# Performance work log

Hardware: AMD Instinct MI355X
Metric: run time of the kernel (lower is better)

## Reference

```python
import jax, jax.numpy as jnp
import numpy as np

HEADS = 8


def setup_inputs() -> dict:
    key = jax.random.key(0)
    ks = jax.random.split(key, 9)
    B, C, H, W = 16, 512, 32, 32
    d = C // HEADS
    scale = d ** -0.5
    return {
        "x": jax.random.normal(ks[0], (B, C, H, W), dtype=jnp.float32),
        "Wq": jax.random.normal(ks[1], (C, C), dtype=jnp.float32) * (C ** -0.5),
        "bq": jax.random.normal(ks[2], (C,), dtype=jnp.float32) * 0.02,
        "Wk": jax.random.normal(ks[3], (C, C), dtype=jnp.float32) * (C ** -0.5),
        "bk": jax.random.normal(ks[4], (C,), dtype=jnp.float32) * 0.02,
        "Wv": jax.random.normal(ks[5], (C, C), dtype=jnp.float32) * (C ** -0.5),
        "bv": jax.random.normal(ks[6], (C,), dtype=jnp.float32) * 0.02,
        "rel_h": jax.random.normal(ks[7], (d, H, 1), dtype=jnp.float32) * scale,
        "rel_w": jax.random.normal(ks[8], (d, 1, W), dtype=jnp.float32) * scale,
    }


def reference(x, Wq, bq, Wk, bk, Wv, bv, rel_h, rel_w):
    B, C, H, W = x.shape
    heads = HEADS
    d = C // heads
    scale = d ** -0.5
    N = H * W
    xf = x.reshape(B, C, N)  # 1x1 conv == per-pixel linear over channels
    q = (jnp.einsum('oc,bcn->bon', Wq, xf) + bq[:, None]).reshape(B, heads, d, N)
    k = (jnp.einsum('oc,bcn->bon', Wk, xf) + bk[:, None]).reshape(B, heads, d, N)
    v = (jnp.einsum('oc,bcn->bon', Wv, xf) + bv[:, None]).reshape(B, heads, d, N)
    q = q * scale
    # content-content scores [B, heads, N, N]
    cc = jnp.einsum('bhdi,bhdj->bhij', q, k)
    # relative position bias table [d, N], projected by q
    cp_tab = (rel_h + rel_w).reshape(d, N)
    cp = jnp.einsum('bhdi,dj->bhij', q, cp_tab)
    beta = jax.nn.softmax(cc + cp, axis=-1)
    attn = jnp.einsum('bhij,bhdj->bhid', beta, v)  # [B, heads, N, d]
    # original does .view(x.shape) on [b,h,i,d] -> keep same raw reshape
    return attn.reshape(B, C, H, W)
```

## Files before the change

kernel.cpp:

```cpp
#include <hip/hip_runtime.h>
#include <hip/hip_bf16.h>
#include <stdint.h>

typedef unsigned short u16;
typedef u16 u16x8 __attribute__((ext_vector_type(8)));
typedef u16 u16x4 __attribute__((ext_vector_type(4)));
typedef __bf16 bf16x8 __attribute__((ext_vector_type(8)));
typedef float f32x4 __attribute__((ext_vector_type(4)));

#define MFMA16(a, b, c) __builtin_amdgcn_mfma_f32_16x16x32_bf16((a), (b), (c), 0, 0, 0)

#define SCALE_Q 0.18033688011112042f

__device__ __forceinline__ u16 f2b(float f) {
    union { float f; unsigned u; } v; v.f = f;
    unsigned r = v.u + 0x7FFFu + ((v.u >> 16) & 1u);
    return (u16)(r >> 16);
}
__device__ __forceinline__ u16 f2b_h(float f) {
    union { float f; unsigned u; } v; v.f = f;
    return (u16)((v.u + 0x8000u) >> 16);
}

__global__ __launch_bounds__(256) void prep(
    const float* __restrict__ x,
    const float* __restrict__ Wq, const float* __restrict__ Wk,
    const float* __restrict__ Wv,
    u16* __restrict__ wb, u16* __restrict__ xT) {
    __shared__ __align__(16) u16 Ls[128 * 72];
    const int tid = threadIdx.x;

    if (blockIdx.x < 384) {
        int g = blockIdx.x * 256 + tid;
        int which = g >> 15;
        const float* src = which == 0 ? Wq : (which == 1 ? Wk : Wv);
        int off = (g & 32767) * 8;
        f32x4 a = *(const f32x4*)(src + off);
        f32x4 b = *(const f32x4*)(src + off + 4);
        u16x8 o;
#pragma unroll
        for (int i = 0; i < 4; ++i) { o[i] = f2b_h(a[i]); o[4 + i] = f2b_h(b[i]); }
        *(u16x8*)(wb + (size_t)g * 8) = o;
        return;
    }

    const int bid = blockIdx.x - 384;
    const int b  = bid >> 6;
    const int ct = (bid >> 3) & 7;
    const int nt = bid & 7;
    const int C0 = ct * 64, N0 = nt * 128;
    const float* xb = x + ((size_t)b << 19);

#pragma unroll
    for (int rep = 0; rep < 4; ++rep) {
        int id = tid + rep * 256;
        int oct = id >> 7, n = id & 127;
        const float* xp = xb + (size_t)(C0 + oct * 8) * 1024 + N0 + n;
        u16x8 xv;
#pragma unroll
        for (int k = 0; k < 8; ++k) xv[k] = f2b_h(xp[k * 1024]);
        *(u16x8*)(Ls + n * 72 + oct * 8) = xv;
    }
    __syncthreads();
#pragma unroll
    for (int rep = 0; rep < 4; ++rep) {
        int id = tid + rep * 256;
        int n = id >> 3, c8 = id & 7;
        *(u16x8*)(xT + ((size_t)b << 19) + (size_t)(N0 + n) * 512 + C0 + c8 * 8) =
            *(u16x8*)(Ls + n * 72 + c8 * 8);
    }
}

__global__ __launch_bounds__(256, 3) void qkv_proj(
    const u16* __restrict__ xT, const u16* __restrict__ wb,
    const float* __restrict__ bq, const float* __restrict__ bk,
    const float* __restrict__ bv,
    const float* __restrict__ rel_h, const float* __restrict__ rel_w,
    u16* __restrict__ qws, u16* __restrict__ kws, u16* __restrict__ vws) {
    __shared__ __align__(16) u16 Xs[128 * 72];
    __shared__ __align__(16) u16 Ws[128 * 72];

    const int tid  = threadIdx.x;
    const int wave = tid >> 6, lane = tid & 63;
    const int quad = lane >> 4, l16 = lane & 15;
    const int wr = wave >> 1, wc = wave & 1;

    const int id = blockIdx.x;
    const int nt = id & 7;
    const int r  = id >> 3;
    const int o0 = r & 3;
    const int r2 = r >> 2;
    const int mm = r2 % 3;
    const int b  = r2 / 3;
    const int N0 = nt * 128;
    const int O0 = o0 * 128;

    const u16*   W    = wb + (size_t)mm * 262144;
    const float* bias = mm == 0 ? bq : (mm == 1 ? bk : bv);
    const u16*   Xb   = xT + ((size_t)b << 19);

    const int sr = tid >> 3, sc8 = tid & 7;

    u16x8 xr[4], wrg[4];
#pragma unroll
    for (int rp = 0; rp < 4; ++rp) {
        xr[rp]  = *(const u16x8*)(Xb + (size_t)(N0 + sr + rp * 32) * 512 + sc8 * 8);
        wrg[rp] = *(const u16x8*)(W  + (size_t)(O0 + sr + rp * 32) * 512 + sc8 * 8);
    }

    f32x4 acc[4][4] = {};

    for (int kt = 0; kt < 8; ++kt) {
        __syncthreads();
#pragma unroll
        for (int rp = 0; rp < 4; ++rp) {
            *(u16x8*)(Xs + (sr + rp * 32) * 72 + sc8 * 8) = xr[rp];
            *(u16x8*)(Ws + (sr + rp * 32) * 72 + sc8 * 8) = wrg[rp];
        }
        __syncthreads();
        if (kt < 7) {
            int c0 = (kt + 1) * 64;
#pragma unroll
            for (int rp = 0; rp < 4; ++rp) {
                xr[rp]  = *(const u16x8*)(Xb + (size_t)(N0 + sr + rp * 32) * 512 + c0 + sc8 * 8);
                wrg[rp] = *(const u16x8*)(W  + (size_t)(O0 + sr + rp * 32) * 512 + c0 + sc8 * 8);
            }
        }
#pragma unroll
        for (int kk = 0; kk < 2; ++kk) {
            bf16x8 af[4], bfr[4];
#pragma unroll
            for (int mi = 0; mi < 4; ++mi)
                af[mi] = *(bf16x8*)(Xs + (wr * 64 + mi * 16 + l16) * 72 + kk * 32 + quad * 8);
#pragma unroll
            for (int ni = 0; ni < 4; ++ni)
                bfr[ni] = *(bf16x8*)(Ws + (wc * 64 + ni * 16 + l16) * 72 + kk * 32 + quad * 8);
#pragma unroll
            for (int mi = 0; mi < 4; ++mi)
#pragma unroll
                for (int ni = 0; ni < 4; ++ni)
                    acc[mi][ni] = MFMA16(af[mi], bfr[ni], acc[mi][ni]);
        }
    }

#pragma unroll
    for (int mi = 0; mi < 4; ++mi) {
#pragma unroll
        for (int ni = 0; ni < 4; ++ni) {
            int o  = O0 + wc * 64 + ni * 16 + l16;
            int h  = o >> 6, dd = o & 63;
            size_t bh = (size_t)b * 8 + h;
            float bv_ = bias[o];
            int n0 = N0 + wr * 64 + mi * 16 + quad * 4;
            if (mm == 2) {
                u16x4 pk;
#pragma unroll
                for (int rr = 0; rr < 4; ++rr) pk[rr] = f2b(acc[mi][ni][rr] + bv_);
                *(u16x4*)(vws + (bh * 64 + dd) * 1024 + n0) = pk;
            } else if (mm == 0) {
#pragma unroll
                for (int rr = 0; rr < 4; ++rr)
                    qws[(bh * 1024 + (n0 + rr)) * 64 + dd] =
                        f2b((acc[mi][ni][rr] + bv_) * SCALE_Q);
            } else {
                float th = rel_h[dd * 32 + (n0 >> 5)];
                f32x4 tw = *(const f32x4*)(rel_w + dd * 32 + (n0 & 31));
#pragma unroll
                for (int rr = 0; rr < 4; ++rr)
                    kws[(bh * 1024 + n0 + rr) * 64 + dd] =
                        f2b(acc[mi][ni][rr] + bv_ + th + tw[rr]);
            }
        }
    }
}

__global__ __launch_bounds__(256, 4) void attn(
    const u16* __restrict__ qws, const u16* __restrict__ kws,
    const u16* __restrict__ vws, float* __restrict__ out) {
    __shared__ __align__(16) u16 KP[64 * 72];
    __shared__ __align__(16) u16 Vt[64 * 72];
    __shared__ __align__(16) u16 Pb[4 * 32 * 68];

    const int tid  = threadIdx.x;
    const int wave = tid >> 6, lane = tid & 63;
    const int quad = lane >> 4, l16 = lane & 15;
    const int id = blockIdx.x;
    const int h  = id & 7;
    const int qt = (id >> 3) & 7;
    const int b  = id >> 6;
    const size_t bh = (size_t)b * 8 + h;

    const u16* Q = qws + (bh * 1024 + (size_t)qt * 128) * 64;
    const u16* K = kws + bh * 1024 * 64;
    const u16* V = vws + bh * 64 * 1024;

    const int srow = tid >> 3, sc8 = tid & 7;

    bf16x8 qf[2][2];
#pragma unroll
    for (int ni = 0; ni < 2; ++ni)
#pragma unroll
        for (int ks = 0; ks < 2; ++ks)
            qf[ni][ks] = *(const bf16x8*)(Q + (wave * 32 + ni * 16 + l16) * 64 + ks * 32 + quad * 8);

    f32x4 accO[4][2] = {};
    f32x4 s4[2] = {};
    u16* Pw = Pb + wave * 2176;

    u16x8 kr0, kr1, vr0, vr1;
    kr0 = *(const u16x8*)(K + (size_t)srow * 64 + sc8 * 8);
    kr1 = *(const u16x8*)(K + (size_t)(srow + 32) * 64 + sc8 * 8);
    vr0 = *(const u16x8*)(V + ((size_t)srow << 10) + sc8 * 8);
    vr1 = *(const u16x8*)(V + ((size_t)(srow + 32) << 10) + sc8 * 8);

    for (int jt = 0; jt < 16; ++jt) {
        __syncthreads();
        *(u16x8*)(KP + srow * 72 + sc8 * 8)        = kr0;
        *(u16x8*)(KP + (srow + 32) * 72 + sc8 * 8) = kr1;
        *(u16x8*)(Vt + srow * 72 + sc8 * 8)        = vr0;
        *(u16x8*)(Vt + (srow + 32) * 72 + sc8 * 8) = vr1;
        __syncthreads();

        if (jt < 15) {
            const u16* Kn = K + (size_t)(jt + 1) * 64 * 64;
            const u16* Vn = V + (size_t)(jt + 1) * 64;
            kr0 = *(const u16x8*)(Kn + (size_t)srow * 64 + sc8 * 8);
            kr1 = *(const u16x8*)(Kn + (size_t)(srow + 32) * 64 + sc8 * 8);
            vr0 = *(const u16x8*)(Vn + ((size_t)srow << 10) + sc8 * 8);
            vr1 = *(const u16x8*)(Vn + ((size_t)(srow + 32) << 10) + sc8 * 8);
        }

        f32x4 accST[4][2] = {};
#pragma unroll
        for (int ks = 0; ks < 2; ++ks) {
            bf16x8 kf[4];
#pragma unroll
            for (int mj = 0; mj < 4; ++mj)
                kf[mj] = *(bf16x8*)(KP + (mj * 16 + l16) * 72 + ks * 32 + quad * 8);
#pragma unroll
            for (int mj = 0; mj < 4; ++mj)
#pragma unroll
                for (int ni = 0; ni < 2; ++ni)
                    accST[mj][ni] = MFMA16(kf[mj], qf[ni][ks], accST[mj][ni]);
        }
#pragma unroll
        for (int ni = 0; ni < 2; ++ni)
#pragma unroll
            for (int mj = 0; mj < 4; ++mj) {
                f32x4 p;
#pragma unroll
                for (int rr = 0; rr < 4; ++rr)
                    p[rr] = __builtin_amdgcn_exp2f(accST[mj][ni][rr]);
                s4[ni] += p;
                u16x4 pk;
#pragma unroll
                for (int rr = 0; rr < 4; ++rr) pk[rr] = f2b_h(p[rr]);
                *(u16x4*)(Pw + (ni * 16 + l16) * 68 + mj * 16 + quad * 4) = pk;
            }
#pragma unroll
        for (int ks2 = 0; ks2 < 2; ++ks2) {
            bf16x8 vf[4], pf[2];
#pragma unroll
            for (int md = 0; md < 4; ++md)
                vf[md] = *(bf16x8*)(Vt + (md * 16 + l16) * 72 + ks2 * 32 + quad * 8);
#pragma unroll
            for (int ni = 0; ni < 2; ++ni)
                pf[ni] = *(bf16x8*)(Pw + (ni * 16 + l16) * 68 + ks2 * 32 + quad * 8);
#pragma unroll
            for (int md = 0; md < 4; ++md)
#pragma unroll
                for (int ni = 0; ni < 2; ++ni)
                    accO[md][ni] = MFMA16(vf[md], pf[ni], accO[md][ni]);
        }
    }

#pragma unroll
    for (int ni = 0; ni < 2; ++ni) {
        float rs = (s4[ni][0] + s4[ni][1]) + (s4[ni][2] + s4[ni][3]);
        rs += __shfl_xor(rs, 16);
        rs += __shfl_xor(rs, 32);
        float inv = 1.0f / rs;
        int i = qt * 128 + wave * 32 + ni * 16 + l16;
#pragma unroll
        for (int md = 0; md < 4; ++md) {
            f32x4 pk;
#pragma unroll
            for (int rr = 0; rr < 4; ++rr) pk[rr] = accO[md][ni][rr] * inv;
            int dd = md * 16 + quad * 4;
            *(f32x4*)(out + (bh * 1024 + i) * 64 + dd) = pk;
        }
    }
}

extern "C" void kernel_launch(void* const* d_in, const int* in_sizes, int n_in,
                              void* d_out, int out_size, void* d_ws, size_t ws_size,
                              hipStream_t stream) {
    const float* x  = (const float*)d_in[0];
    const float* Wq = (const float*)d_in[1];
    const float* bq = (const float*)d_in[2];
    const float* Wk = (const float*)d_in[3];
    const float* bk = (const float*)d_in[4];
    const float* Wv = (const float*)d_in[5];
    const float* bv = (const float*)d_in[6];
    const float* rh = (const float*)d_in[7];
    const float* rw = (const float*)d_in[8];
    float* out = (float*)d_out;

    u16* kws = (u16*)d_ws;
    u16* vws = kws + 8388608;
    u16* qws = vws + 8388608;
    u16* wb  = qws + 8388608;
    u16* xT  = (u16*)d_out;

    prep<<<1408, 256, 0, stream>>>(x, Wq, Wk, Wv, wb, xT);
    qkv_proj<<<1536, 256, 0, stream>>>(xT, wb, bq, bk, bv, rh, rw, qws, kws, vws);
    attn<<<1024, 256, 0, stream>>>(qws, kws, vws, out);
}
```

Baseline: 201.4 us.

## Keep softmax probabilities in registers via permuted V layout, double-buffer K/V LDS

```diff
diff --git a/kernel.cpp b/kernel.cpp
--- a/kernel.cpp
+++ b/kernel.cpp
@@ -156,7 +156,9 @@
                 u16x4 pk;
 #pragma unroll
                 for (int rr = 0; rr < 4; ++rr) pk[rr] = f2b(acc[mi][ni][rr] + bv_);
-                *(u16x4*)(vws + (bh * 64 + dd) * 1024 + n0) = pk;
+                int qq = (n0 >> 2) & 3, ss = (n0 >> 4) & 1;
+                int np = (n0 & ~31) | (qq * 8 + ss * 4);
+                *(u16x4*)(vws + (bh * 64 + dd) * 1024 + np) = pk;
             } else if (mm == 0) {
 #pragma unroll
                 for (int rr = 0; rr < 4; ++rr)
@@ -177,9 +179,8 @@
 __global__ __launch_bounds__(256, 4) void attn(
     const u16* __restrict__ qws, const u16* __restrict__ kws,
     const u16* __restrict__ vws, float* __restrict__ out) {
-    __shared__ __align__(16) u16 KP[64 * 72];
-    __shared__ __align__(16) u16 Vt[64 * 72];
-    __shared__ __align__(16) u16 Pb[4 * 32 * 68];
+    __shared__ __align__(16) u16 KPb[2][64 * 72];
+    __shared__ __align__(16) u16 Vtb[2][64 * 72];
 
     const int tid  = threadIdx.x;
     const int wave = tid >> 6, lane = tid & 63;
@@ -205,7 +206,6 @@
 
     f32x4 accO[4][2] = {};
     f32x4 s4[2] = {};
-    u16* Pw = Pb + wave * 2176;
 
     u16x8 kr0, kr1, vr0, vr1;
     kr0 = *(const u16x8*)(K + (size_t)srow * 64 + sc8 * 8);
@@ -214,7 +214,8 @@
     vr1 = *(const u16x8*)(V + ((size_t)(srow + 32) << 10) + sc8 * 8);
 
     for (int jt = 0; jt < 16; ++jt) {
-        __syncthreads();
+        u16* KP = KPb[jt & 1];
+        u16* Vt = Vtb[jt & 1];
         *(u16x8*)(KP + srow * 72 + sc8 * 8)        = kr0;
         *(u16x8*)(KP + (srow + 32) * 72 + sc8 * 8) = kr1;
         *(u16x8*)(Vt + srow * 72 + sc8 * 8)        = vr0;
@@ -237,40 +238,54 @@
 #pragma unroll
             for (int mj = 0; mj < 4; ++mj)
                 kf[mj] = *(bf16x8*)(KP + (mj * 16 + l16) * 72 + ks * 32 + quad * 8);
+            __builtin_amdgcn_s_setprio(1);
 #pragma unroll
             for (int mj = 0; mj < 4; ++mj)
 #pragma unroll
                 for (int ni = 0; ni < 2; ++ni)
                     accST[mj][ni] = MFMA16(kf[mj], qf[ni][ks], accST[mj][ni]);
-        }
-#pragma unroll
-        for (int ni = 0; ni < 2; ++ni)
-#pragma unroll
-            for (int mj = 0; mj < 4; ++mj) {
+            __builtin_amdgcn_s_setprio(0);
+        }
+
+#pragma unroll
+        for (int mj = 0; mj < 4; ++mj)
+#pragma unroll
+            for (int ni = 0; ni < 2; ++ni) {
                 f32x4 p;
 #pragma unroll
                 for (int rr = 0; rr < 4; ++rr)
                     p[rr] = __builtin_amdgcn_exp2f(accST[mj][ni][rr]);
                 s4[ni] += p;
-                u16x4 pk;
-#pragma unroll
-                for (int rr = 0; rr < 4; ++rr) pk[rr] = f2b_h(p[rr]);
-                *(u16x4*)(Pw + (ni * 16 + l16) * 68 + mj * 16 + quad * 4) = pk;
+                accST[mj][ni] = p;
             }
+
+        union pkun { u16x8 u; bf16x8 b; } pfr[2][2];
+#pragma unroll
+        for (int ks2 = 0; ks2 < 2; ++ks2)
+#pragma unroll
+            for (int ni = 0; ni < 2; ++ni) {
+                u16x8 t;
+#pragma unroll
+                for (int rr = 0; rr < 4; ++rr) {
+                    t[rr]     = f2b_h(accST[2 * ks2][ni][rr]);
+                    t[4 + rr] = f2b_h(accST[2 * ks2 + 1][ni][rr]);
+                }
+                pfr[ks2][ni].u = t;
+            }
+
 #pragma unroll
         for (int ks2 = 0; ks2 < 2; ++ks2) {
-            bf16x8 vf[4], pf[2];
+            bf16x8 vf[4];
 #pragma unroll
             for (int md = 0; md < 4; ++md)
                 vf[md] = *(bf16x8*)(Vt + (md * 16 + l16) * 72 + ks2 * 32 + quad * 8);
-#pragma unroll
-            for (int ni = 0; ni < 2; ++ni)
-                pf[ni] = *(bf16x8*)(Pw + (ni * 16 + l16) * 68 + ks2 * 32 + quad * 8);
+            __builtin_amdgcn_s_setprio(1);
 #pragma unroll
             for (int md = 0; md < 4; ++md)
 #pragma unroll
                 for (int ni = 0; ni < 2; ++ni)
-                    accO[md][ni] = MFMA16(vf[md], pf[ni], accO[md][ni]);
+                    accO[md][ni] = MFMA16(vf[md], pfr[ks2][ni].b, accO[md][ni]);
+            __builtin_amdgcn_s_setprio(0);
         }
     }
 
```

Measured after the change: 204.3 us. Within noise of the previous version (+1.5%).
